# Kernel tuning notes

Measured on AMD Instinct MI355X. Metric: run time of the kernel, lower is better.

The kernel has to match this reference:

```python
import jax, jax.numpy as jnp
import numpy as np
from jax.scipy.special import logsumexp

E = 512      # input_size (= 2*hidden_size)
T = 24       # output_size (num CRF tags)
B, S = 32, 512
HEADS = 2


def setup_inputs() -> dict:
    key = jax.random.key(0)
    ks = jax.random.split(key, 12)
    u = lambda k, shape, a: jax.random.uniform(k, shape, jnp.float32, -a, a)
    inp = {
        "encoder_outputs": jax.random.normal(ks[0], (B, S, E), jnp.float32),
        "labels": jax.random.randint(ks[1], (B, S), 0, T),
        "mask": jnp.ones((B, S), dtype=bool),
        # nn.MultiheadAttention params
        "Win": u(ks[2], (3 * E, E), E ** -0.5),
        "bin_": jnp.zeros((3 * E,), jnp.float32),
        "Wout": u(ks[3], (E, E), E ** -0.5),
        "bout": jnp.zeros((E,), jnp.float32),
        # crf_linear
        "crf_w": u(ks[4], (T, E), E ** -0.5),
        "crf_b": u(ks[5], (T,), E ** -0.5),
        # torchcrf CRF params (uniform(-0.1, 0.1))
        "start_t": u(ks[6], (T,), 0.1),
        "end_t": u(ks[7], (T,), 0.1),
        "trans": u(ks[8], (T, T), 0.1),
        # entity_linear
        "ent_w": u(ks[9], (2, E), E ** -0.5),
        "ent_b": u(ks[10], (2,), E ** -0.5),
    }
    return inp


def _mha(x, Win, bin_, Wout, bout):
    b, s, e = x.shape
    hd = e // HEADS
    qkv = x @ Win.T + bin_                       # [B,S,3E]
    q, k, v = jnp.split(qkv, 3, axis=-1)
    q = q.reshape(b, s, HEADS, hd)
    k = k.reshape(b, s, HEADS, hd)
    v = v.reshape(b, s, HEADS, hd)
    scores = jnp.einsum("bqhd,bkhd->bhqk", q, k) / jnp.sqrt(jnp.float32(hd))
    attn = jax.nn.softmax(scores, axis=-1)       # [B,H,S,S]
    out = jnp.einsum("bhqk,bkhd->bqhd", attn, v).reshape(b, s, e)
    return out @ Wout.T + bout


def _crf_numerator(em, labels, maskf, start_t, end_t, trans):
    # em: [B,S,T] emissions, labels: [B,S] int, maskf: [B,S] float (mask[:,0]==1)
    bidx = jnp.arange(em.shape[0])
    score = start_t[labels[:, 0]] + em[bidx, 0, labels[:, 0]]
    prev, cur = labels[:, :-1], labels[:, 1:]
    em_t = jnp.take_along_axis(em[:, 1:], cur[:, :, None], axis=2)[..., 0]
    score = score + ((trans[prev, cur] + em_t) * maskf[:, 1:]).sum(axis=1)
    seq_ends = maskf.sum(axis=1).astype(jnp.int32) - 1
    last_tags = labels[bidx, seq_ends]
    return score + end_t[last_tags]


def _crf_normalizer(em, maskf, start_t, end_t, trans):
    score0 = start_t + em[:, 0]                  # [B,T]

    def step(score, x):
        e_t, m_t = x                             # [B,T], [B]
        nxt = logsumexp(score[:, :, None] + trans[None] + e_t[:, None, :], axis=1)
        return jnp.where(m_t[:, None] > 0, nxt, score), None

    xs = (em[:, 1:].swapaxes(0, 1), maskf[:, 1:].T)
    score, _ = jax.lax.scan(step, score0, xs)
    return logsumexp(score + end_t, axis=1)


def _viterbi(em, start_t, end_t, trans):
    # decode is called without a mask -> mask of all ones
    score0 = start_t + em[:, 0]                  # [B,T]

    def step(score, e_t):
        nxt = score[:, :, None] + trans[None] + e_t[:, None, :]  # [B,T,T]
        return nxt.max(axis=1), nxt.argmax(axis=1)

    score, history = jax.lax.scan(step, score0, em[:, 1:].swapaxes(0, 1))
    last = jnp.argmax(score + end_t, axis=1)     # [B]

    def back(tag, hist):
        prev = jnp.take_along_axis(hist, tag[:, None], axis=1)[:, 0]
        return prev, prev

    _, prevs = jax.lax.scan(back, last, history, reverse=True)  # [S-1,B]
    return jnp.concatenate([prevs, last[None]], axis=0).T       # [B,S]


def reference(encoder_outputs, labels, mask, Win, bin_, Wout, bout,
              crf_w, crf_b, start_t, end_t, trans, ent_w, ent_b):
    attn = _mha(encoder_outputs, Win, bin_, Wout, bout)
    dec = jax.nn.relu(attn)                      # [B,S,E]
    fc_out = dec @ crf_w.T + crf_b               # [B,S,T]
    maskf = mask.astype(fc_out.dtype)
    num = _crf_numerator(fc_out, labels, maskf, start_t, end_t, trans)
    den = _crf_normalizer(fc_out, maskf, start_t, end_t, trans)
    llh = (num - den).sum() / maskf.sum()        # reduction='token_mean'
    crf_out = _viterbi(fc_out, start_t, end_t, trans)
    seg_out = jax.nn.log_softmax(dec @ ent_w.T + ent_b, axis=2)
    return crf_out, seg_out, -llh
```

## Files before the change

kernel.cpp:

```cpp
#include <hip/hip_runtime.h>

#define BB 32
#define SS 512
#define EE 512
#define NHH 2
#define HDD 256
#define E3 1536
#define NT 24
#define MR (BB*SS)

typedef _Float16 half8  __attribute__((ext_vector_type(8)));
typedef _Float16 half4v __attribute__((ext_vector_type(4)));
typedef float    f32x4  __attribute__((ext_vector_type(4)));

__device__ __forceinline__ float rl(float v, int l) {
    return __int_as_float(__builtin_amdgcn_readlane(__float_as_int(v), l));
}

template<int BN>
__global__ __launch_bounds__(256) void mfma_gemm(
    const float* __restrict__ A, int lda, long sAhi, long sAlo, int zA,
    const float* __restrict__ B, int ldb, long sBhi, long sBlo, int zB,
    const float* __restrict__ bias,
    float* __restrict__ C, int ldc, long sChi, long sClo, int zC,
    int K, int relu)
{
    __shared__ __align__(16) _Float16 sAh[8*640];
    __shared__ __align__(16) _Float16 sAl[8*640];
    __shared__ __align__(16) _Float16 sBh[8*640];
    __shared__ __align__(16) _Float16 sBl[8*640];

    const int t = threadIdx.x;
    const int z = blockIdx.z;
    const int za = zA + z, zb = zB + z, zc = zC + z;
    const float* Ab = A + (size_t)(za>>1)*sAhi + (size_t)(za&1)*sAlo
                        + (size_t)blockIdx.y*128*lda;
    const float* Bb = B + (size_t)(zb>>1)*sBhi + (size_t)(zb&1)*sBlo
                        + (BN ? (size_t)blockIdx.x*128
                              : (size_t)blockIdx.x*128*ldb);

    const int wv = t >> 6, lane = t & 63;
    const int wm = wv >> 1, wn = wv & 1;
    const int lm = lane & 15, lq = lane >> 4;

    f32x4 acc[4][4];
#pragma unroll
    for (int i = 0; i < 4; ++i)
#pragma unroll
        for (int j = 0; j < 4; ++j) acc[i][j] = (f32x4){0.f,0.f,0.f,0.f};

    const int r8  = t >> 3;
    const int kc  = (t & 7) * 4;
    const int bnn4 = (t & 31) * 4;
    const int bnk4 = (t >> 5) * 4;

    for (int k0 = 0; k0 < K; k0 += 32) {
        float4 ga[4], gb[4]; float4 gv4[4];
#pragma unroll
        for (int i = 0; i < 4; ++i)
            ga[i] = *(const float4*)(Ab + (size_t)(r8 + 32*i)*lda + k0 + kc);
        if (BN) {
#pragma unroll
            for (int kk = 0; kk < 4; ++kk)
                gv4[kk] = *(const float4*)(Bb + (size_t)(k0 + bnk4 + kk)*ldb + bnn4);
        } else {
#pragma unroll
            for (int i = 0; i < 4; ++i)
                gb[i] = *(const float4*)(Bb + (size_t)(r8 + 32*i)*ldb + k0 + kc);
        }
        __syncthreads();
#pragma unroll
        for (int i = 0; i < 4; ++i) {
            const int row  = r8 + 32*i;
            const int base = (row >> 4)*640 + (row & 15)*40 + kc;
            float4 a = ga[i];
            _Float16 h0 = (_Float16)a.x, h1 = (_Float16)a.y,
                     h2 = (_Float16)a.z, h3 = (_Float16)a.w;
            _Float16 l0 = (_Float16)(a.x - (float)h0),
                     l1 = (_Float16)(a.y - (float)h1),
                     l2 = (_Float16)(a.z - (float)h2),
                     l3 = (_Float16)(a.w - (float)h3);
            *(half4v*)&sAh[base] = (half4v){h0,h1,h2,h3};
            *(half4v*)&sAl[base] = (half4v){l0,l1,l2,l3};
        }
        if (BN) {
#pragma unroll
            for (int kk = 0; kk < 4; ++kk) {
                const float vv[4] = {gv4[kk].x, gv4[kk].y, gv4[kk].z, gv4[kk].w};
#pragma unroll
                for (int nn = 0; nn < 4; ++nn) {
                    const int n = bnn4 + nn;
                    float v = vv[nn];
                    _Float16 h = (_Float16)v;
                    _Float16 l = (_Float16)(v - (float)h);
                    const int base = (n >> 4)*640 + (n & 15)*40 + bnk4 + kk;
                    sBh[base] = h;
                    sBl[base] = l;
                }
            }
        } else {
#pragma unroll
            for (int i = 0; i < 4; ++i) {
                const int row  = r8 + 32*i;
                const int base = (row >> 4)*640 + (row & 15)*40 + kc;
                float4 b = gb[i];
                _Float16 h0 = (_Float16)b.x, h1 = (_Float16)b.y,
                         h2 = (_Float16)b.z, h3 = (_Float16)b.w;
                _Float16 l0 = (_Float16)(b.x - (float)h0),
                         l1 = (_Float16)(b.y - (float)h1),
                         l2 = (_Float16)(b.z - (float)h2),
                         l3 = (_Float16)(b.w - (float)h3);
                *(half4v*)&sBh[base] = (half4v){h0,h1,h2,h3};
                *(half4v*)&sBl[base] = (half4v){l0,l1,l2,l3};
            }
        }
        __syncthreads();

        half8 bhf[4], blf[4];
#pragma unroll
        for (int j = 0; j < 4; ++j) {
            const int tb = (wn*4 + j)*640 + lm*40 + lq*8;
            bhf[j] = *(const half8*)&sBh[tb];
            blf[j] = *(const half8*)&sBl[tb];
        }
#pragma unroll
        for (int i = 0; i < 4; ++i) {
            const int ta = (wm*4 + i)*640 + lm*40 + lq*8;
            half8 ah = *(const half8*)&sAh[ta];
            half8 al = *(const half8*)&sAl[ta];
#pragma unroll
            for (int j = 0; j < 4; ++j) {
                acc[i][j] = __builtin_amdgcn_mfma_f32_16x16x32_f16(ah, bhf[j], acc[i][j], 0, 0, 0);
                acc[i][j] = __builtin_amdgcn_mfma_f32_16x16x32_f16(al, bhf[j], acc[i][j], 0, 0, 0);
                acc[i][j] = __builtin_amdgcn_mfma_f32_16x16x32_f16(ah, blf[j], acc[i][j], 0, 0, 0);
            }
        }
    }

    float* Cb = C + (size_t)(zc>>1)*sChi + (size_t)(zc&1)*sClo;
#pragma unroll
    for (int j = 0; j < 4; ++j) {
        const int col = blockIdx.x*128 + (wn*4 + j)*16 + lm;
        const float bj = bias ? bias[col] : 0.f;
#pragma unroll
        for (int i = 0; i < 4; ++i) {
            const int row0 = blockIdx.y*128 + (wm*4 + i)*16 + lq*4;
#pragma unroll
            for (int r = 0; r < 4; ++r) {
                float v = acc[i][j][r] + bj;
                if (relu) v = fmaxf(v, 0.f);
                Cb[(size_t)(row0 + r)*ldc + col] = v;
            }
        }
    }
}

__global__ __launch_bounds__(256) void softmax_rows(float* __restrict__ scores)
{
    const int w    = threadIdx.x >> 6;
    const int lane = threadIdx.x & 63;
    const size_t row = (size_t)blockIdx.x * 4 + w;
    float* p = scores + row * SS + lane * 8;
    float4 v0 = *(float4*)(p);
    float4 v1 = *(float4*)(p + 4);
    const float scale = 0.0625f;
    float m = fmaxf(fmaxf(fmaxf(v0.x, v0.y), fmaxf(v0.z, v0.w)),
                    fmaxf(fmaxf(v1.x, v1.y), fmaxf(v1.z, v1.w)));
#pragma unroll
    for (int off = 32; off >= 1; off >>= 1) m = fmaxf(m, __shfl_xor(m, off));
    v0.x = __expf((v0.x - m) * scale); v0.y = __expf((v0.y - m) * scale);
    v0.z = __expf((v0.z - m) * scale); v0.w = __expf((v0.w - m) * scale);
    v1.x = __expf((v1.x - m) * scale); v1.y = __expf((v1.y - m) * scale);
    v1.z = __expf((v1.z - m) * scale); v1.w = __expf((v1.w - m) * scale);
    float sum = v0.x + v0.y + v0.z + v0.w + v1.x + v1.y + v1.z + v1.w;
#pragma unroll
    for (int off = 32; off >= 1; off >>= 1) sum += __shfl_xor(sum, off);
    float inv = 1.f / sum;
    v0.x *= inv; v0.y *= inv; v0.z *= inv; v0.w *= inv;
    v1.x *= inv; v1.y *= inv; v1.z *= inv; v1.w *= inv;
    *(float4*)(p)     = v0;
    *(float4*)(p + 4) = v1;
}

__global__ __launch_bounds__(192) void fc_crf_kernel(
    const float* __restrict__ dec, const float* __restrict__ W,
    const float* __restrict__ bias, float* __restrict__ out)
{
    __shared__ __align__(16) float Ws[NT][516];
    for (int i = threadIdx.x; i < NT*128; i += 192) {
        int j = i >> 7, c = (i & 127) * 4;
        *(float4*)&Ws[j][c] = *(const float4*)(W + (size_t)j*EE + c);
    }
    __syncthreads();
    const int t = threadIdx.x;
    const int rloc = t / NT;
    const int j = t - rloc * NT;
    const int row = blockIdx.x * 8 + rloc;
    const float4* a = (const float4*)(dec + (size_t)row * EE);
    float acc = 0.f;
#pragma unroll 4
    for (int i = 0; i < 128; ++i) {
        float4 x = a[i];
        float4 y = *(const float4*)&Ws[j][i*4];
        acc += x.x*y.x + x.y*y.y + x.z*y.z + x.w*y.w;
    }
    out[(size_t)row * NT + j] = acc + bias[j];
}

__global__ __launch_bounds__(64, 1) void crf_seg_kernel(
    const float* __restrict__ fc, const int* __restrict__ labels,
    const float* __restrict__ start_t, const float* __restrict__ end_t,
    const float* __restrict__ trans, const float* __restrict__ dec,
    const float* __restrict__ ent_w, const float* __restrict__ ent_b,
    float* __restrict__ num, float* __restrict__ den,
    float* __restrict__ crf_out, float* __restrict__ segout)
{
    __shared__ __align__(16) float fc_lds[SS*NT];
    __shared__ unsigned char hist[(SS-1)*NT];
    __shared__ unsigned char anchor[SS];

    const int blk  = blockIdx.x;
    const int lane = threadIdx.x;

    if (blk >= 96) {
        const int row0 = (blk - 96) * 8;
        const float4* w0 = (const float4*)(ent_w);
        const float4* w1 = (const float4*)(ent_w + EE);
        const int i0 = lane * 2, i1 = lane * 2 + 1;
        const float4 u0 = w0[i0], u1 = w0[i1];
        const float4 q0 = w1[i0], q1 = w1[i1];
        const float eb0 = ent_b[0], eb1 = ent_b[1];
#pragma unroll 2
        for (int r = 0; r < 8; ++r) {
            const int row = row0 + r;
            const float4* a = (const float4*)(dec + (size_t)row * EE);
            float acc0 = 0.f, acc1 = 0.f;
            {
                float4 x = a[i0];
                acc0 += x.x*u0.x + x.y*u0.y + x.z*u0.z + x.w*u0.w;
                acc1 += x.x*q0.x + x.y*q0.y + x.z*q0.z + x.w*q0.w;
            }
            {
                float4 x = a[i1];
                acc0 += x.x*u1.x + x.y*u1.y + x.z*u1.z + x.w*u1.w;
                acc1 += x.x*q1.x + x.y*q1.y + x.z*q1.z + x.w*q1.w;
            }
#pragma unroll
            for (int off = 32; off >= 1; off >>= 1) {
                acc0 += __shfl_xor(acc0, off);
                acc1 += __shfl_xor(acc1, off);
            }
            if (lane == 0) {
                float l0 = acc0 + eb0;
                float l1 = acc1 + eb1;
                float m  = fmaxf(l0, l1);
                float lse = m + __logf(__expf(l0 - m) + __expf(l1 - m));
                segout[(size_t)row*2 + 0] = l0 - lse;
                segout[(size_t)row*2 + 1] = l1 - lse;
            }
        }
        return;
    }

    const int role = blk >> 5;
    const int b    = blk & 31;
    const float* fcb = fc + (size_t)b * SS * NT;

    if (role == 2) {
        float acc = 0.f;
        for (int s = 1 + lane; s < SS; s += 64) {
            int prev = labels[b*SS + s - 1];
            int cur  = labels[b*SS + s];
            acc += trans[prev*NT + cur] + fcb[(size_t)s*NT + cur];
        }
        if (lane == 0) {
            int l0 = labels[b*SS];
            acc += start_t[l0] + fcb[l0] + end_t[labels[b*SS + SS - 1]];
        }
#pragma unroll
        for (int off = 32; off >= 1; off >>= 1) acc += __shfl_xor(acc, off);
        if (lane == 0) num[b] = acc;
        return;
    }

#pragma unroll
    for (int i = 0; i < SS*NT/256; ++i) {
        const int idx = i*256 + lane*4;
        *(float4*)&fc_lds[idx] = *(const float4*)(fcb + idx);
    }
    __syncthreads();

    const int j = (lane < NT) ? lane : 0;

    if (role == 0) {
        float sc = start_t[j] + fc_lds[j];
        float etr[NT];
#pragma unroll
        for (int i = 0; i < NT; ++i) etr[i] = __expf(trans[i*NT + j]);
        float em_next = fc_lds[NT + j];
        for (int s = 1; s < SS; ++s) {
            float em = em_next;
            int snx = (s + 1 < SS) ? s + 1 : s;
            em_next = fc_lds[snx * NT + j];
            const float m  = __builtin_amdgcn_readfirstlane(sc);
            const float eo = __expf(sc - m);
            float a0 = 0.f, a1 = 0.f, a2 = 0.f, a3 = 0.f;
#pragma unroll
            for (int i = 0; i < NT; i += 4) {
                a0 = fmaf(rl(eo, i+0), etr[i+0], a0);
                a1 = fmaf(rl(eo, i+1), etr[i+1], a1);
                a2 = fmaf(rl(eo, i+2), etr[i+2], a2);
                a3 = fmaf(rl(eo, i+3), etr[i+3], a3);
            }
            sc = m + __logf((a0 + a1) + (a2 + a3)) + em;
        }
        float v = (lane < NT) ? sc + end_t[j] : -1e30f;
        float m2 = v;
#pragma unroll
        for (int off = 32; off >= 1; off >>= 1) m2 = fmaxf(m2, __shfl_xor(m2, off));
        float e = (lane < NT) ? __expf(v - m2) : 0.f;
#pragma unroll
        for (int off = 32; off >= 1; off >>= 1) e += __shfl_xor(e, off);
        if (lane == 0) den[b] = m2 + __logf(e);
    } else {
        const int jj   = lane & 31;
        const int jc   = (jj < NT) ? jj : 0;
        const int half = lane >> 5;
        const int cb   = half * 12;

        float trC[12];
#pragma unroll
        for (int ii = 0; ii < 12; ++ii) trC[ii] = trans[(cb + ii)*NT + jc];

        float sc = start_t[jc] + fc_lds[jc];
        float em_next = fc_lds[NT + jc];
        for (int s = 1; s < SS; ++s) {
            float em = em_next;
            int snx = (s + 1 < SS) ? s + 1 : s;
            em_next = fc_lds[snx * NT + jc];
            float tv[12]; int ti[12];
#pragma unroll
            for (int ii = 0; ii < 12; ++ii) {
                tv[ii] = __shfl(sc, cb + ii) + trC[ii];
                ti[ii] = cb + ii;
            }
#pragma unroll
            for (int st = 1; st < 12; st <<= 1)
#pragma unroll
                for (int i = 0; i + st < 12; i += 2*st)
                    if (tv[i+st] > tv[i]) { tv[i] = tv[i+st]; ti[i] = ti[i+st]; }
            float ov = __shfl_xor(tv[0], 32);
            int   oi = __shfl_xor(ti[0], 32);
            float bv = tv[0]; int bi2 = ti[0];
            if (ov > bv || (ov == bv && oi < bi2)) { bv = ov; bi2 = oi; }
            sc = bv + em;
            if (lane < NT) hist[(s-1)*NT + lane] = (unsigned char)bi2;
        }
        float bv = (lane < NT) ? sc + end_t[jc] : -1e30f;
        int bi = (lane < NT) ? lane : NT;
#pragma unroll
        for (int off = 32; off >= 1; off >>= 1) {
            float ov = __shfl_xor(bv, off);
            int   oi = __shfl_xor(bi, off);
            if (ov > bv || (ov == bv && oi < bi)) { bv = ov; bi = oi; }
        }
        __syncthreads();

        unsigned char* C0 = hist;
        unsigned char* C1 = (unsigned char*)fc_lds;
        if (lane < 48) {
            const int t24 = (lane < 24) ? lane : lane - 24;
            const int h0c = (lane < 24) ? 1 : 3;
#pragma unroll 4
            for (int k = 0; k < 128; ++k) {
                int h = h0c + 4*k;
                if (h <= 509) {
                    int u = C0[(h+1)*NT + t24];
                    C1[h*NT + t24] = C0[h*NT + u];
                }
            }
        }
        __syncthreads();
        if (lane == 0) {
            int tg = bi;
            anchor[SS-1] = (unsigned char)tg;
            for (int h = SS-3; h >= 1; h -= 2) {
                tg = C1[h*NT + tg];
                anchor[h] = (unsigned char)tg;
            }
        }
        __syncthreads();
        for (int s = lane; s < SS; s += 64) {
            int tag;
            if (s == SS-1)      tag = anchor[SS-1];
            else if (s & 1)     tag = anchor[s];
            else                tag = C0[s*NT + anchor[s+1]];
            crf_out[(size_t)b*SS + s] = (float)tag;
        }
    }
}

__global__ __launch_bounds__(64) void llh_kernel(
    const float* __restrict__ num, const float* __restrict__ den,
    float* __restrict__ out)
{
    int t = threadIdx.x;
    float v = (t < BB) ? (num[t] - den[t]) : 0.f;
#pragma unroll
    for (int off = 32; off >= 1; off >>= 1) v += __shfl_xor(v, off);
    if (t == 0) out[(size_t)MR * 3] = -(v / (float)MR);
}

extern "C" void kernel_launch(void* const* d_in, const int* in_sizes, int n_in,
                              void* d_out, int out_size, void* d_ws, size_t ws_size,
                              hipStream_t stream) {
    const float* enc     = (const float*)d_in[0];
    const int*   labels  = (const int*)  d_in[1];
    const float* Win     = (const float*)d_in[3];
    const float* bin     = (const float*)d_in[4];
    const float* Wout    = (const float*)d_in[5];
    const float* bout    = (const float*)d_in[6];
    const float* crf_w   = (const float*)d_in[7];
    const float* crf_b   = (const float*)d_in[8];
    const float* start_t = (const float*)d_in[9];
    const float* end_t   = (const float*)d_in[10];
    const float* trans   = (const float*)d_in[11];
    const float* ent_w   = (const float*)d_in[12];
    const float* ent_b   = (const float*)d_in[13];
    float* out = (float*)d_out;

    float* ws   = (float*)d_ws;
    float* qkv  = ws;
    float* attn = qkv  + (size_t)MR * E3;
    float* big  = attn + (size_t)MR * EE;
    float* sch  = big;
    float* dec  = big;
    float* fc   = big  + (size_t)MR * EE;
    float* num  = fc   + (size_t)MR * NT;
    float* den  = num  + BB;

    dim3 blk(256);
    mfma_gemm<0><<<dim3(E3/128, MR/128, 1), blk, 0, stream>>>(
        enc, EE, 0, 0, 0,  Win, EE, 0, 0, 0,  bin,
        qkv, E3, 0, 0, 0,  EE, 0);
    for (int p = 0; p < 2; ++p) {
        int zoff = p * 32;
        mfma_gemm<0><<<dim3(SS/128, SS/128, 32), blk, 0, stream>>>(
            qkv,      E3, (long)SS*E3, HDD, zoff,
            qkv + EE, E3, (long)SS*E3, HDD, zoff,
            nullptr,
            sch, SS, 2L*SS*SS, (long)SS*SS, 0,
            HDD, 0);
        softmax_rows<<<(32*SS)/4, blk, 0, stream>>>(sch);
        mfma_gemm<1><<<dim3(HDD/128, SS/128, 32), blk, 0, stream>>>(
            sch, SS, 2L*SS*SS, (long)SS*SS, 0,
            qkv + 2*EE, E3, (long)SS*E3, HDD, zoff,
            nullptr,
            attn, EE, (long)SS*EE, HDD, zoff,
            SS, 0);
    }
    mfma_gemm<0><<<dim3(EE/128, MR/128, 1), blk, 0, stream>>>(
        attn, EE, 0, 0, 0,  Wout, EE, 0, 0, 0,  bout,
        dec, EE, 0, 0, 0,  EE, 1);
    fc_crf_kernel<<<MR/8, dim3(192), 0, stream>>>(dec, crf_w, crf_b, fc);
    crf_seg_kernel<<<96 + MR/8, dim3(64), 0, stream>>>(
        fc, labels, start_t, end_t, trans, dec, ent_w, ent_b,
        num, den, out, out + MR);
    llh_kernel<<<1, 64, 0, stream>>>(num, den, out);
}
```

Baseline: 573.8 us.

## Prefetch next K-tile global loads into registers during MFMA compute

```diff
diff --git a/kernel.cpp b/kernel.cpp
--- a/kernel.cpp
+++ b/kernel.cpp
@@ -54,20 +54,28 @@
     const int bnn4 = (t & 31) * 4;
     const int bnk4 = (t >> 5) * 4;
 
+    auto loadA = [&](float4 g[4], int kk0) {
+#pragma unroll
+        for (int i = 0; i < 4; ++i)
+            g[i] = *(const float4*)(Ab + (size_t)(r8 + 32*i)*lda + kk0 + kc);
+    };
+    auto loadB = [&](float4 g[4], int kk0) {
+        if (BN) {
+#pragma unroll
+            for (int kk = 0; kk < 4; ++kk)
+                g[kk] = *(const float4*)(Bb + (size_t)(kk0 + bnk4 + kk)*ldb + bnn4);
+        } else {
+#pragma unroll
+            for (int i = 0; i < 4; ++i)
+                g[i] = *(const float4*)(Bb + (size_t)(r8 + 32*i)*ldb + kk0 + kc);
+        }
+    };
+
+    float4 ga[4], gb[4];
+    loadA(ga, 0);
+    loadB(gb, 0);
+
     for (int k0 = 0; k0 < K; k0 += 32) {
-        float4 ga[4], gb[4]; float4 gv4[4];
-#pragma unroll
-        for (int i = 0; i < 4; ++i)
-            ga[i] = *(const float4*)(Ab + (size_t)(r8 + 32*i)*lda + k0 + kc);
-        if (BN) {
-#pragma unroll
-            for (int kk = 0; kk < 4; ++kk)
-                gv4[kk] = *(const float4*)(Bb + (size_t)(k0 + bnk4 + kk)*ldb + bnn4);
-        } else {
-#pragma unroll
-            for (int i = 0; i < 4; ++i)
-                gb[i] = *(const float4*)(Bb + (size_t)(r8 + 32*i)*ldb + k0 + kc);
-        }
         __syncthreads();
 #pragma unroll
         for (int i = 0; i < 4; ++i) {
@@ -84,19 +92,25 @@
             *(half4v*)&sAl[base] = (half4v){l0,l1,l2,l3};
         }
         if (BN) {
+            float vv[4][4];
 #pragma unroll
             for (int kk = 0; kk < 4; ++kk) {
-                const float vv[4] = {gv4[kk].x, gv4[kk].y, gv4[kk].z, gv4[kk].w};
-#pragma unroll
-                for (int nn = 0; nn < 4; ++nn) {
-                    const int n = bnn4 + nn;
-                    float v = vv[nn];
-                    _Float16 h = (_Float16)v;
-                    _Float16 l = (_Float16)(v - (float)h);
-                    const int base = (n >> 4)*640 + (n & 15)*40 + bnk4 + kk;
-                    sBh[base] = h;
-                    sBl[base] = l;
+                vv[kk][0] = gb[kk].x; vv[kk][1] = gb[kk].y;
+                vv[kk][2] = gb[kk].z; vv[kk][3] = gb[kk].w;
+            }
+#pragma unroll
+            for (int nn = 0; nn < 4; ++nn) {
+                const int n = bnn4 + nn;
+                half4v h, l;
+#pragma unroll
+                for (int kk = 0; kk < 4; ++kk) {
+                    _Float16 hh = (_Float16)vv[kk][nn];
+                    h[kk] = hh;
+                    l[kk] = (_Float16)(vv[kk][nn] - (float)hh);
                 }
+                const int base = (n >> 4)*640 + (n & 15)*40 + bnk4;
+                *(half4v*)&sBh[base] = h;
+                *(half4v*)&sBl[base] = l;
             }
         } else {
 #pragma unroll
@@ -116,6 +130,13 @@
         }
         __syncthreads();
 
+        float4 gan[4], gbn[4];
+        const bool more = (k0 + 32 < K);
+        if (more) {
+            loadA(gan, k0 + 32);
+            loadB(gbn, k0 + 32);
+        }
+
         half8 bhf[4], blf[4];
 #pragma unroll
         for (int j = 0; j < 4; ++j) {
@@ -134,6 +155,11 @@
                 acc[i][j] = __builtin_amdgcn_mfma_f32_16x16x32_f16(al, bhf[j], acc[i][j], 0, 0, 0);
                 acc[i][j] = __builtin_amdgcn_mfma_f32_16x16x32_f16(ah, blf[j], acc[i][j], 0, 0, 0);
             }
+        }
+
+        if (more) {
+#pragma unroll
+            for (int i = 0; i < 4; ++i) { ga[i] = gan[i]; gb[i] = gbn[i]; }
         }
     }
 
```

After: 565.6 us. About the same (-1.4%).

## Pre-split GEMM operands into fp16 hi/lo planes and prefetch next K tile

Applied to the files above, without the earlier changes.

```diff
diff --git a/kernel.cpp b/kernel.cpp
--- a/kernel.cpp
+++ b/kernel.cpp
@@ -17,12 +17,30 @@
     return __int_as_float(__builtin_amdgcn_readlane(__float_as_int(v), l));
 }
 
-template<int BN>
+__global__ __launch_bounds__(256) void presplit(
+    const float* __restrict__ in, _Float16* __restrict__ oh,
+    _Float16* __restrict__ ol, int n4)
+{
+    int i = blockIdx.x * 256 + threadIdx.x;
+    const int stride = gridDim.x * 256;
+    for (; i < n4; i += stride) {
+        float4 v = ((const float4*)in)[i];
+        half4v h, l;
+        h[0] = (_Float16)v.x; l[0] = (_Float16)(v.x - (float)h[0]);
+        h[1] = (_Float16)v.y; l[1] = (_Float16)(v.y - (float)h[1]);
+        h[2] = (_Float16)v.z; l[2] = (_Float16)(v.z - (float)h[2]);
+        h[3] = (_Float16)v.w; l[3] = (_Float16)(v.w - (float)h[3]);
+        ((half4v*)oh)[i] = h;
+        ((half4v*)ol)[i] = l;
+    }
+}
+
+template<int MODE, int EPI>
 __global__ __launch_bounds__(256) void mfma_gemm(
-    const float* __restrict__ A, int lda, long sAhi, long sAlo, int zA,
-    const float* __restrict__ B, int ldb, long sBhi, long sBlo, int zB,
+    const void* A_, const void* A2_, int lda, long sAhi, long sAlo, int zA,
+    const void* B_, const void* B2_, int ldb, long sBhi, long sBlo, int zB,
     const float* __restrict__ bias,
-    float* __restrict__ C, int ldc, long sChi, long sClo, int zC,
+    void* C_, void* C2_, int ldc, long sChi, long sClo, int zC,
     int K, int relu)
 {
     __shared__ __align__(16) _Float16 sAh[8*640];
@@ -33,11 +51,6 @@
     const int t = threadIdx.x;
     const int z = blockIdx.z;
     const int za = zA + z, zb = zB + z, zc = zC + z;
-    const float* Ab = A + (size_t)(za>>1)*sAhi + (size_t)(za&1)*sAlo
-                        + (size_t)blockIdx.y*128*lda;
-    const float* Bb = B + (size_t)(zb>>1)*sBhi + (size_t)(zb&1)*sBlo
-                        + (BN ? (size_t)blockIdx.x*128
-                              : (size_t)blockIdx.x*128*ldb);
 
     const int wv = t >> 6, lane = t & 63;
     const int wm = wv >> 1, wn = wv & 1;
@@ -49,72 +62,98 @@
 #pragma unroll
         for (int j = 0; j < 4; ++j) acc[i][j] = (f32x4){0.f,0.f,0.f,0.f};
 
+    const int r4  = t >> 2;
+    const int kc8 = (t & 3) * 8;
     const int r8  = t >> 3;
     const int kc  = (t & 7) * 4;
-    const int bnn4 = (t & 31) * 4;
-    const int bnk4 = (t >> 5) * 4;
+    const int tt    = t & 127;
+    const int nIdx8 = (tt >> 3) * 8;
+    const int kIdx4 = (tt & 7) * 4;
+    const bool loPlane = (t < 128);
+
+    const _Float16 *Ah = nullptr, *Al = nullptr, *Bh = nullptr, *Bl = nullptr;
+    const float *Af = nullptr;
+    const _Float16 *Vh = nullptr, *Vl = nullptr;
+    if constexpr (MODE == 0) {
+        const size_t aoff = (size_t)(za>>1)*sAhi + (size_t)(za&1)*sAlo
+                          + (size_t)blockIdx.y*128*lda;
+        Ah = (const _Float16*)A_  + aoff;
+        Al = (const _Float16*)A2_ + aoff;
+        const size_t boff = (size_t)(zb>>1)*sBhi + (size_t)(zb&1)*sBlo
+                          + (size_t)blockIdx.x*128*ldb;
+        Bh = (const _Float16*)B_  + boff;
+        Bl = (const _Float16*)B2_ + boff;
+    } else {
+        Af = (const float*)A_ + (size_t)(za>>1)*sAhi + (size_t)(za&1)*sAlo
+           + (size_t)blockIdx.y*128*lda;
+        const size_t boff = (size_t)(zb>>1)*sBhi + (size_t)(zb&1)*sBlo
+                          + (size_t)blockIdx.x*128;
+        Vh = (const _Float16*)B_  + boff;
+        Vl = (const _Float16*)B2_ + boff;
+    }
+
+    half8 pA[4], pB[4];
+    float4 ga[4];
+    half8 vb[4];
+
+    auto load_tile = [&](int kk0) {
+        if constexpr (MODE == 0) {
+            pA[0] = *(const half8*)(Ah + (size_t)r4*lda + kk0 + kc8);
+            pA[1] = *(const half8*)(Ah + (size_t)(r4+64)*lda + kk0 + kc8);
+            pA[2] = *(const half8*)(Al + (size_t)r4*lda + kk0 + kc8);
+            pA[3] = *(const half8*)(Al + (size_t)(r4+64)*lda + kk0 + kc8);
+            pB[0] = *(const half8*)(Bh + (size_t)r4*ldb + kk0 + kc8);
+            pB[1] = *(const half8*)(Bh + (size_t)(r4+64)*ldb + kk0 + kc8);
+            pB[2] = *(const half8*)(Bl + (size_t)r4*ldb + kk0 + kc8);
+            pB[3] = *(const half8*)(Bl + (size_t)(r4+64)*ldb + kk0 + kc8);
+        } else {
+#pragma unroll
+            for (int i = 0; i < 4; ++i)
+                ga[i] = *(const float4*)(Af + (size_t)(r8 + 32*i)*lda + kk0 + kc);
+            const _Float16* Vsel = loPlane ? Vh : Vl;
+#pragma unroll
+            for (int kk = 0; kk < 4; ++kk)
+                vb[kk] = *(const half8*)(Vsel + (size_t)(kk0 + kIdx4 + kk)*ldb + nIdx8);
+        }
+    };
+
+    load_tile(0);
 
     for (int k0 = 0; k0 < K; k0 += 32) {
-        float4 ga[4], gb[4]; float4 gv4[4];
-#pragma unroll
-        for (int i = 0; i < 4; ++i)
-            ga[i] = *(const float4*)(Ab + (size_t)(r8 + 32*i)*lda + k0 + kc);
-        if (BN) {
-#pragma unroll
-            for (int kk = 0; kk < 4; ++kk)
-                gv4[kk] = *(const float4*)(Bb + (size_t)(k0 + bnk4 + kk)*ldb + bnn4);
-        } else {
-#pragma unroll
-            for (int i = 0; i < 4; ++i)
-                gb[i] = *(const float4*)(Bb + (size_t)(r8 + 32*i)*ldb + k0 + kc);
-        }
         __syncthreads();
-#pragma unroll
-        for (int i = 0; i < 4; ++i) {
-            const int row  = r8 + 32*i;
-            const int base = (row >> 4)*640 + (row & 15)*40 + kc;
-            float4 a = ga[i];
-            _Float16 h0 = (_Float16)a.x, h1 = (_Float16)a.y,
-                     h2 = (_Float16)a.z, h3 = (_Float16)a.w;
-            _Float16 l0 = (_Float16)(a.x - (float)h0),
-                     l1 = (_Float16)(a.y - (float)h1),
-                     l2 = (_Float16)(a.z - (float)h2),
-                     l3 = (_Float16)(a.w - (float)h3);
-            *(half4v*)&sAh[base] = (half4v){h0,h1,h2,h3};
-            *(half4v*)&sAl[base] = (half4v){l0,l1,l2,l3};
-        }
-        if (BN) {
-#pragma unroll
-            for (int kk = 0; kk < 4; ++kk) {
-                const float vv[4] = {gv4[kk].x, gv4[kk].y, gv4[kk].z, gv4[kk].w};
-#pragma unroll
-                for (int nn = 0; nn < 4; ++nn) {
-                    const int n = bnn4 + nn;
-                    float v = vv[nn];
-                    _Float16 h = (_Float16)v;
-                    _Float16 l = (_Float16)(v - (float)h);
-                    const int base = (n >> 4)*640 + (n & 15)*40 + bnk4 + kk;
-                    sBh[base] = h;
-                    sBl[base] = l;
-                }
-            }
+        if constexpr (MODE == 0) {
+            const int a0 = (r4>>4)*640 + (r4&15)*40 + kc8;
+            const int a1 = a0 + 4*640;
+            *(half8*)&sAh[a0] = pA[0]; *(half8*)&sAh[a1] = pA[1];
+            *(half8*)&sAl[a0] = pA[2]; *(half8*)&sAl[a1] = pA[3];
+            *(half8*)&sBh[a0] = pB[0]; *(half8*)&sBh[a1] = pB[1];
+            *(half8*)&sBl[a0] = pB[2]; *(half8*)&sBl[a1] = pB[3];
         } else {
 #pragma unroll
             for (int i = 0; i < 4; ++i) {
                 const int row  = r8 + 32*i;
                 const int base = (row >> 4)*640 + (row & 15)*40 + kc;
-                float4 b = gb[i];
-                _Float16 h0 = (_Float16)b.x, h1 = (_Float16)b.y,
-                         h2 = (_Float16)b.z, h3 = (_Float16)b.w;
-                _Float16 l0 = (_Float16)(b.x - (float)h0),
-                         l1 = (_Float16)(b.y - (float)h1),
-                         l2 = (_Float16)(b.z - (float)h2),
-                         l3 = (_Float16)(b.w - (float)h3);
-                *(half4v*)&sBh[base] = (half4v){h0,h1,h2,h3};
-                *(half4v*)&sBl[base] = (half4v){l0,l1,l2,l3};
+                float4 a = ga[i];
+                _Float16 h0 = (_Float16)a.x, h1 = (_Float16)a.y,
+                         h2 = (_Float16)a.z, h3 = (_Float16)a.w;
+                _Float16 l0 = (_Float16)(a.x - (float)h0),
+                         l1 = (_Float16)(a.y - (float)h1),
+                         l2 = (_Float16)(a.z - (float)h2),
+                         l3 = (_Float16)(a.w - (float)h3);
+                *(half4v*)&sAh[base] = (half4v){h0,h1,h2,h3};
+                *(half4v*)&sAl[base] = (half4v){l0,l1,l2,l3};
+            }
+            _Float16* dstp = loPlane ? sBh : sBl;
+#pragma unroll
+            for (int nn = 0; nn < 8; ++nn) {
+                const int n = nIdx8 + nn;
+                half4v w = { vb[0][nn], vb[1][nn], vb[2][nn], vb[3][nn] };
+                *(half4v*)&dstp[(n>>4)*640 + (n&15)*40 + kIdx4] = w;
             }
         }
         __syncthreads();
+
+        if (k0 + 32 < K) load_tile(k0 + 32);
 
         half8 bhf[4], blf[4];
 #pragma unroll
@@ -137,19 +176,41 @@
         }
     }
 
-    float* Cb = C + (size_t)(zc>>1)*sChi + (size_t)(zc&1)*sClo;
-#pragma unroll
-    for (int j = 0; j < 4; ++j) {
-        const int col = blockIdx.x*128 + (wn*4 + j)*16 + lm;
-        const float bj = bias ? bias[col] : 0.f;
-#pragma unroll
-        for (int i = 0; i < 4; ++i) {
-            const int row0 = blockIdx.y*128 + (wm*4 + i)*16 + lq*4;
-#pragma unroll
-            for (int r = 0; r < 4; ++r) {
-                float v = acc[i][j][r] + bj;
-                if (relu) v = fmaxf(v, 0.f);
-                Cb[(size_t)(row0 + r)*ldc + col] = v;
+    if constexpr (EPI == 0) {
+        float* Cb = (float*)C_ + (size_t)(zc>>1)*sChi + (size_t)(zc&1)*sClo;
+#pragma unroll
+        for (int j = 0; j < 4; ++j) {
+            const int col = blockIdx.x*128 + (wn*4 + j)*16 + lm;
+            const float bj = bias ? bias[col] : 0.f;
+#pragma unroll
+            for (int i = 0; i < 4; ++i) {
+                const int row0 = blockIdx.y*128 + (wm*4 + i)*16 + lq*4;
+#pragma unroll
+                for (int r = 0; r < 4; ++r) {
+                    float v = acc[i][j][r] + bj;
+                    if (relu) v = fmaxf(v, 0.f);
+                    Cb[(size_t)(row0 + r)*ldc + col] = v;
+                }
+            }
+        }
+    } else {
+        _Float16* Ch = (_Float16*)C_  + (size_t)(zc>>1)*sChi + (size_t)(zc&1)*sClo;
+        _Float16* Cl = (_Float16*)C2_ + (size_t)(zc>>1)*sChi + (size_t)(zc&1)*sClo;
+#pragma unroll
+        for (int j = 0; j < 4; ++j) {
+            const int col = blockIdx.x*128 + (wn*4 + j)*16 + lm;
+            const float bj = bias ? bias[col] : 0.f;
+#pragma unroll
+            for (int i = 0; i < 4; ++i) {
+                const int row0 = blockIdx.y*128 + (wm*4 + i)*16 + lq*4;
+#pragma unroll
+                for (int r = 0; r < 4; ++r) {
+                    float v = acc[i][j][r] + bj;
+                    _Float16 h = (_Float16)v;
+                    _Float16 l = (_Float16)(v - (float)h);
+                    Ch[(size_t)(row0 + r)*ldc + col] = h;
+                    Cl[(size_t)(row0 + r)*ldc + col] = l;
+                }
             }
         }
     }
@@ -429,39 +490,50 @@
     const float* ent_b   = (const float*)d_in[13];
     float* out = (float*)d_out;
 
-    float* ws   = (float*)d_ws;
-    float* qkv  = ws;
-    float* attn = qkv  + (size_t)MR * E3;
-    float* big  = attn + (size_t)MR * EE;
-    float* sch  = big;
-    float* dec  = big;
-    float* fc   = big  + (size_t)MR * EE;
-    float* num  = fc   + (size_t)MR * NT;
-    float* den  = num  + BB;
+    char* p = (char*)d_ws;
+    _Float16* qkvh = (_Float16*)p; p += (size_t)MR*E3*2;
+    _Float16* qkvl = (_Float16*)p; p += (size_t)MR*E3*2;
+    float*    big  = (float*)p;    p += (size_t)MR*EE*4;
+    float*    fc   = (float*)p;    p += (size_t)MR*NT*4;
+    float*    num  = (float*)p;    p += BB*4;
+    float*    den  = (float*)p;    p += BB*4;
+    _Float16* ench = (_Float16*)p; p += (size_t)MR*EE*2;
+    _Float16* encl = (_Float16*)p; p += (size_t)MR*EE*2;
+    _Float16* Winh = (_Float16*)p; p += (size_t)E3*EE*2;
+    _Float16* Winl = (_Float16*)p; p += (size_t)E3*EE*2;
+    _Float16* Wouth= (_Float16*)p; p += (size_t)EE*EE*2;
+    _Float16* Woutl= (_Float16*)p; p += (size_t)EE*EE*2;
+    float* sch = big;
+    float* dec = big;
+    _Float16* attnh = ench;
+    _Float16* attnl = encl;
 
     dim3 blk(256);
-    mfma_gemm<0><<<dim3(E3/128, MR/128, 1), blk, 0, stream>>>(
-        enc, EE, 0, 0, 0,  Win, EE, 0, 0, 0,  bin,
-        qkv, E3, 0, 0, 0,  EE, 0);
-    for (int p = 0; p < 2; ++p) {
-        int zoff = p * 32;
-        mfma_gemm<0><<<dim3(SS/128, SS/128, 32), blk, 0, stream>>>(
-            qkv,      E3, (long)SS*E3, HDD, zoff,
-            qkv + EE, E3, (long)SS*E3, HDD, zoff,
+    presplit<<<1024, blk, 0, stream>>>(enc,  ench,  encl,  MR*EE/4);
+    presplit<<<512,  blk, 0, stream>>>(Win,  Winh,  Winl,  E3*EE/4);
+    presplit<<<256,  blk, 0, stream>>>(Wout, Wouth, Woutl, EE*EE/4);
+    mfma_gemm<0,1><<<dim3(E3/128, MR/128, 1), blk, 0, stream>>>(
+        ench, encl, EE, 0, 0, 0,  Winh, Winl, EE, 0, 0, 0,  bin,
+        qkvh, qkvl, E3, 0, 0, 0,  EE, 0);
+    for (int pz = 0; pz < 2; ++pz) {
+        int zoff = pz * 32;
+        mfma_gemm<0,0><<<dim3(SS/128, SS/128, 32), blk, 0, stream>>>(
+            qkvh,      qkvl,      E3, (long)SS*E3, HDD, zoff,
+            qkvh + EE, qkvl + EE, E3, (long)SS*E3, HDD, zoff,
             nullptr,
-            sch, SS, 2L*SS*SS, (long)SS*SS, 0,
+            sch, nullptr, SS, 2L*SS*SS, (long)SS*SS, 0,
             HDD, 0);
         softmax_rows<<<(32*SS)/4, blk, 0, stream>>>(sch);
-        mfma_gemm<1><<<dim3(HDD/128, SS/128, 32), blk, 0, stream>>>(
-            sch, SS, 2L*SS*SS, (long)SS*SS, 0,
-            qkv + 2*EE, E3, (long)SS*E3, HDD, zoff,
+        mfma_gemm<1,1><<<dim3(HDD/128, SS/128, 32), blk, 0, stream>>>(
+            sch, nullptr, SS, 2L*SS*SS, (long)SS*SS, 0,
+            qkvh + 2*EE, qkvl + 2*EE, E3, (long)SS*E3, HDD, zoff,
             nullptr,
-            attn, EE, (long)SS*EE, HDD, zoff,
+            attnh, attnl, EE, (long)SS*EE, HDD, zoff,
             SS, 0);
     }
-    mfma_gemm<0><<<dim3(EE/128, MR/128, 1), blk, 0, stream>>>(
-        attn, EE, 0, 0, 0,  Wout, EE, 0, 0, 0,  bout,
-        dec, EE, 0, 0, 0,  EE, 1);
+    mfma_gemm<0,0><<<dim3(EE/128, MR/128, 1), blk, 0, stream>>>(
+        attnh, attnl, EE, 0, 0, 0,  Wouth, Woutl, EE, 0, 0, 0,  bout,
+        dec, nullptr, EE, 0, 0, 0,  EE, 1);
     fc_crf_kernel<<<MR/8, dim3(192), 0, stream>>>(dec, crf_w, crf_b, fc);
     crf_seg_kernel<<<96 + MR/8, dim3(64), 0, stream>>>(
         fc, labels, start_t, end_t, trans, dec, ent_w, ent_b,
```

After: 587.4 us. +2.4%, slower.
